# Kernel tuning notes

Measured on AMD Instinct MI355X. Metric: run time of the kernel, lower is better.

## Reference

```python
import jax, jax.numpy as jnp
import numpy as np
import math

B, C, H, W = 2, 64, 64, 64
DI = 2 * C          # d_inner
N = 16              # d_state
R = math.ceil(C / 16)  # dt_rank
K = 3               # d_conv
L = H * W

PARAM_KEYS = [
    'pe_x_w', 'pe_x_b', 'rms_x_w', 'conv_x_w', 'conv_x_b',
    'pe_info_w', 'pe_info_b', 'rms_info_w', 'conv_info_w', 'conv_info_b',
    'pe_mask_w', 'pe_mask_b', 'rms_mask_w', 'conv_mask_w', 'conv_mask_b',
    'in_x_w', 'in_info_w', 'in_mask_w',
    'delta_w', 'dt_w', 'dt_b', 'B_w', 'C_w', 'A_log', 'out_w',
]


def setup_inputs():
    key = jax.random.key(0)
    ki = iter(jax.random.split(key, 40))
    def nrm(shape, scale=1.0):
        return jax.random.normal(next(ki), shape, jnp.float32) * scale
    sc, sdi, sr, sk = 1/np.sqrt(C), 1/np.sqrt(DI), 1/np.sqrt(R), 1/np.sqrt(K)
    inp = {}
    for name in ('up', 'mask', 'x', 'y', 'z'):
        inp[name] = nrm((B, C, H, W))
    for role in ('x', 'info', 'mask'):
        inp[f'pe_{role}_w'] = nrm((3, C, C), sc)
        inp[f'pe_{role}_b'] = jnp.zeros((3, C), jnp.float32)
        inp[f'rms_{role}_w'] = jnp.ones((3, C), jnp.float32)
        inp[f'conv_{role}_w'] = nrm((3, DI, K), sk)
        inp[f'conv_{role}_b'] = nrm((3, DI), sk)
    inp['in_x_w'] = nrm((3, 2 * DI, C), sc)
    inp['in_info_w'] = nrm((3, DI, C), sc)
    inp['in_mask_w'] = nrm((3, DI, C), sc)
    inp['delta_w'] = nrm((3, R, DI), sdi)
    inp['dt_w'] = nrm((3, DI, R), sr)
    rng = np.random.default_rng(0)
    dt = np.exp(rng.uniform(size=(3, DI)) * (np.log(0.1) - np.log(0.001)) + np.log(0.001)).clip(min=1e-4)
    inp['dt_b'] = jnp.asarray(np.log(-np.expm1(-dt)), jnp.float32)
    inp['B_w'] = nrm((3, N, DI), sdi)
    inp['C_w'] = nrm((3, N, DI), sdi)
    inp['A_log'] = jnp.tile(jnp.log(jnp.arange(1, N + 1, dtype=jnp.float32)), (3, DI, 1))
    inp['out_w'] = nrm((3, C, DI), sdi)
    return inp


def embed1x1(t, w, b):
    # PatchEmbed with patch_size=1: 1x1 conv then flatten to [B, L, C]
    y = jnp.einsum('bchw,oc->bohw', t, w) + b[None, :, None, None]
    bb, cc, hh, ww = y.shape
    return y.reshape(bb, cc, hh * ww).transpose(0, 2, 1)


def rms_norm(x, w, eps=1e-5):
    return x * jax.lax.rsqrt(jnp.mean(x * x, axis=-1, keepdims=True) + eps) * w


def causal_dwconv_silu(x, w, b):
    # x [B, D, L]; depthwise causal conv1d (left-pad K-1), then SiLU
    kk = w.shape[1]
    xp = jnp.pad(x, ((0, 0), (0, 0), (kk - 1, 0)))
    y = jax.lax.conv_general_dilated(
        xp, w[:, None, :], window_strides=(1,), padding='VALID',
        dimension_numbers=('NCH', 'OIH', 'NCH'), feature_group_count=w.shape[0])
    return jax.nn.silu(y + b[None, :, None])


def selective_scan(u, delta, A, Bm, Cm):
    # u, delta: [B, D, L]; A: [D, N]; Bm, Cm: [B, N, L]
    dA = jnp.exp(jnp.einsum('bdl,dn->lbdn', delta, A))           # [L,B,D,N]
    dBu = jnp.einsum('bdl,bnl,bdl->lbdn', delta, Bm, u)          # [L,B,D,N]
    Ct = Cm.transpose(2, 0, 1)                                   # [L,B,N]
    h0 = jnp.zeros((u.shape[0], u.shape[1], A.shape[1]), u.dtype)
    def step(h, inp):
        dA_t, dBu_t, C_t = inp
        h = dA_t * h + dBu_t
        return h, jnp.einsum('bdn,bn->bd', h, C_t)
    _, ys = jax.lax.scan(step, h0, (dA, dBu, Ct))
    return ys.transpose(1, 2, 0)                                 # [B,D,L]


def branch(xin, maskin, upin, p):
    bb, cc, hh, ww = xin.shape
    xe = rms_norm(embed1x1(xin, p['pe_x_w'], p['pe_x_b']), p['rms_x_w'])        # [B,L,C]
    xz = jnp.einsum('blc,dc->bdl', xe, p['in_x_w'])                              # [B,2DI,L]
    di = xz.shape[1] // 2
    xc, x_act = xz[:, :di], xz[:, di:]
    info = rms_norm(embed1x1(upin, p['pe_info_w'], p['pe_info_b']), p['rms_info_w'])
    info = jnp.einsum('blc,dc->bdl', info, p['in_info_w'])
    mk = rms_norm(embed1x1(maskin, p['pe_mask_w'], p['pe_mask_b']), p['rms_mask_w'])
    mk = jnp.einsum('blc,dc->bdl', mk, p['in_mask_w'])
    xc = causal_dwconv_silu(xc, p['conv_x_w'], p['conv_x_b'])
    mk = causal_dwconv_silu(mk, p['conv_mask_w'], p['conv_mask_b'])
    info = causal_dwconv_silu(info, p['conv_info_w'], p['conv_info_b'])
    # S6: delta from mask, B from info, C from x
    delta = jnp.einsum('bdl,rd->brl', mk, p['delta_w'])
    delta = jnp.einsum('brl,dr->bdl', delta, p['dt_w'])
    delta = jax.nn.softplus(delta + p['dt_b'][None, :, None])
    A = -jnp.exp(p['A_log'])
    Bm = jnp.einsum('bdl,nd->bnl', info, p['B_w'])
    Cm = jnp.einsum('bdl,nd->bnl', xc, p['C_w'])
    y = selective_scan(xc, delta, A, Bm, Cm)
    y = y * jax.nn.silu(x_act)
    y = jnp.einsum('bdl,cd->blc', y, p['out_w'])
    return y.transpose(0, 2, 1).reshape(bb, cc, hh, ww) + xin


def forward(up, mask, x, y, z, *params):
    pall = dict(zip(PARAM_KEYS, params))
    out = None
    for i, feat in enumerate((x, y, z)):
        p = {k: v[i] for k, v in pall.items()}
        o = branch(feat, mask, up, p)
        out = o if out is None else out + o
    return out


def reference(up, mask, x, y, z,
              pe_x_w, pe_x_b, rms_x_w, conv_x_w, conv_x_b,
              pe_info_w, pe_info_b, rms_info_w, conv_info_w, conv_info_b,
              pe_mask_w, pe_mask_b, rms_mask_w, conv_mask_w, conv_mask_b,
              in_x_w, in_info_w, in_mask_w,
              delta_w, dt_w, dt_b, B_w, C_w, A_log, out_w):
    return forward(up, mask, x, y, z,
                   pe_x_w, pe_x_b, rms_x_w, conv_x_w, conv_x_b,
                   pe_info_w, pe_info_b, rms_info_w, conv_info_w, conv_info_b,
                   pe_mask_w, pe_mask_b, rms_mask_w, conv_mask_w, conv_mask_b,
                   in_x_w, in_info_w, in_mask_w,
                   delta_w, dt_w, dt_b, B_w, C_w, A_log, out_w)
```

## Files before the change

kernel.cpp:

```cpp
#include <hip/hip_runtime.h>
#include <math.h>

namespace {

constexpr int NB = 3;
constexpr int BB = 2;
constexpr int CC = 64;
constexpr int LLEN = 4096;
constexpr int DI = 128;
constexpr int NN = 16;
constexpr int RR = 4;
constexpr int GG = 256;
constexpr int LC = 16;
constexpr int NSEQ = NB * BB * DI * NN;
constexpr size_t SBUF = (size_t)NB * BB * DI * LLEN;

typedef _Float16 f16;
typedef __attribute__((ext_vector_type(4))) float f32x4;
typedef __attribute__((ext_vector_type(8))) short bf16x8;
typedef __attribute__((ext_vector_type(4))) _Float16 f16x4;
typedef __attribute__((ext_vector_type(8))) _Float16 f16x8;

__device__ __forceinline__ float siluf(float v) { return v / (1.f + __expf(-v)); }

__device__ __forceinline__ short cvt_bf16(float f) {
    union { float f; unsigned u; } v; v.f = f;
    unsigned r = v.u + 0x7fffu + ((v.u >> 16) & 1u);
    return (short)(r >> 16);
}
__device__ __forceinline__ unsigned pack_bf16(float lo, float hi) {
    return ((unsigned)(unsigned short)cvt_bf16(hi) << 16) | (unsigned short)cvt_bf16(lo);
}
__device__ __forceinline__ bf16x8 pack8(float4 a, float4 b) {
    bf16x8 r;
    r[0] = cvt_bf16(a.x); r[1] = cvt_bf16(a.y); r[2] = cvt_bf16(a.z); r[3] = cvt_bf16(a.w);
    r[4] = cvt_bf16(b.x); r[5] = cvt_bf16(b.y); r[6] = cvt_bf16(b.z); r[7] = cvt_bf16(b.w);
    return r;
}
__device__ __forceinline__ f16x4 to_h4(float a, float b, float c, float d) {
    f16x4 r; r[0] = (f16)a; r[1] = (f16)b; r[2] = (f16)c; r[3] = (f16)d; return r;
}
__device__ __forceinline__ float4 to_f4(f16x4 v) {
    return make_float4((float)v[0], (float)v[1], (float)v[2], (float)v[3]);
}
__device__ __forceinline__ int swz16(int l, int d) {
    int b = d >> 3;
    int bs = (b & 8) | ((b ^ l) & 7);
    return l * 128 + bs * 8 + (d & 7);
}

__global__ __launch_bounds__(256) void k1_embed(
    const float* __restrict__ up, const float* __restrict__ mask_,
    const float* __restrict__ fx, const float* __restrict__ fy, const float* __restrict__ fz,
    const float* __restrict__ pe_x_w, const float* __restrict__ pe_x_b, const float* __restrict__ rms_x_w,
    const float* __restrict__ pe_i_w, const float* __restrict__ pe_i_b, const float* __restrict__ rms_i_w,
    const float* __restrict__ pe_m_w, const float* __restrict__ pe_m_b, const float* __restrict__ rms_m_w,
    const float* __restrict__ in_x_w, const float* __restrict__ in_i_w, const float* __restrict__ in_m_w,
    f16* __restrict__ xc_pre, f16* __restrict__ x_act,
    f16* __restrict__ info_pre, f16* __restrict__ mk_pre)
{
    __shared__ short sE[64 * 64];
    __shared__ float red[4][64];
    __shared__ float sscl[64];

    int lt = blockIdx.x, job = blockIdx.y, b = blockIdx.z;
    int i = job / 3, r = job % 3;
    const float *src, *pw, *pb, *rw, *iw;
    if (r == 0) {
        src = (i == 0 ? fx : (i == 1 ? fy : fz));
        pw = pe_x_w + i * 4096; pb = pe_x_b + i * 64; rw = rms_x_w + i * 64;
        iw = in_x_w + (size_t)i * 256 * 64;
    } else if (r == 1) {
        src = up;
        pw = pe_i_w + i * 4096; pb = pe_i_b + i * 64; rw = rms_i_w + i * 64;
        iw = in_i_w + (size_t)i * 128 * 64;
    } else {
        src = mask_;
        pw = pe_m_w + i * 4096; pb = pe_m_b + i * 64; rw = rms_m_w + i * 64;
        iw = in_m_w + (size_t)i * 128 * 64;
    }
    int t = threadIdx.x;
    int w = t >> 6, lane = t & 63, lo = lane & 15, hi = lane >> 4;
    int l0 = lt * 64;
    const float* Xg = src + (size_t)b * 64 * LLEN;

    f32x4 acc1[4];
    #pragma unroll
    for (int nt = 0; nt < 4; ++nt) acc1[nt] = (f32x4){0.f, 0.f, 0.f, 0.f};

    #pragma unroll
    for (int ks = 0; ks < 2; ++ks) {
        const float* ap = pw + (16 * w + lo) * 64 + ks * 32 + hi * 8;
        bf16x8 a1 = pack8(*(const float4*)ap, *(const float4*)(ap + 4));
        #pragma unroll
        for (int nt = 0; nt < 4; ++nt) {
            const float* xc = Xg + (size_t)(ks * 32 + hi * 8) * LLEN + l0 + nt * 16 + lo;
            bf16x8 b1;
            #pragma unroll
            for (int j = 0; j < 8; ++j) b1[j] = cvt_bf16(xc[(size_t)j * LLEN]);
            acc1[nt] = __builtin_amdgcn_mfma_f32_16x16x32_bf16(a1, b1, acc1[nt], 0, 0, 0);
        }
    }

    float4 pbv = *(const float4*)&pb[16 * w + 4 * hi];
    float e_[4][4];
    #pragma unroll
    for (int nt = 0; nt < 4; ++nt) {
        e_[nt][0] = acc1[nt][0] + pbv.x;
        e_[nt][1] = acc1[nt][1] + pbv.y;
        e_[nt][2] = acc1[nt][2] + pbv.z;
        e_[nt][3] = acc1[nt][3] + pbv.w;
        float s = e_[nt][0] * e_[nt][0] + e_[nt][1] * e_[nt][1]
                + e_[nt][2] * e_[nt][2] + e_[nt][3] * e_[nt][3];
        s += __shfl_xor(s, 16);
        s += __shfl_xor(s, 32);
        if (lane < 16) red[w][nt * 16 + lo] = s;
    }
    __syncthreads();
    if (t < 64) {
        float s = red[0][t] + red[1][t] + red[2][t] + red[3][t];
        sscl[t] = rsqrtf(s * (1.f / 64.f) + 1e-5f);
    }
    __syncthreads();

    {
        int ob = 2 * w + (hi >> 1);
        #pragma unroll
        for (int nt = 0; nt < 4; ++nt) {
            float sc = sscl[16 * nt + lo];
            unsigned p0 = pack_bf16(e_[nt][0] * sc, e_[nt][1] * sc);
            unsigned p1 = pack_bf16(e_[nt][2] * sc, e_[nt][3] * sc);
            unsigned* p = (unsigned*)&sE[(16 * nt + lo) * 64 + (ob ^ (lo & 7)) * 8 + 4 * (hi & 1)];
            p[0] = p0; p[1] = p1;
        }
    }
    __syncthreads();

    bf16x8 b2[4][2];
    #pragma unroll
    for (int nt = 0; nt < 4; ++nt)
        #pragma unroll
        for (int ks = 0; ks < 2; ++ks) {
            int db = ks * 4 + hi;
            b2[nt][ks] = *(const bf16x8*)&sE[(16 * nt + lo) * 64 + (db ^ (lo & 7)) * 8];
        }

    size_t obase = ((size_t)(i * 2 + b)) * DI * LLEN;
    int MT = (r == 0) ? 4 : 2;
    for (int mm = 0; mm < MT; ++mm) {
        int m = MT * w + mm;
        bf16x8 a2[2];
        #pragma unroll
        for (int ks = 0; ks < 2; ++ks) {
            const float* wp = iw + (size_t)(16 * m + lo) * 64 + ks * 32 + hi * 8;
            float4 w0 = *(const float4*)wp;
            float4 w1 = *(const float4*)(wp + 4);
            float4 r0 = *(const float4*)&rw[ks * 32 + hi * 8];
            float4 r1 = *(const float4*)&rw[ks * 32 + hi * 8 + 4];
            w0.x *= r0.x; w0.y *= r0.y; w0.z *= r0.z; w0.w *= r0.w;
            w1.x *= r1.x; w1.y *= r1.y; w1.z *= r1.z; w1.w *= r1.w;
            a2[ks] = pack8(w0, w1);
        }
        f32x4 acc2[4];
        #pragma unroll
        for (int nt = 0; nt < 4; ++nt) acc2[nt] = (f32x4){0.f, 0.f, 0.f, 0.f};
        #pragma unroll
        for (int ks = 0; ks < 2; ++ks)
            #pragma unroll
            for (int nt = 0; nt < 4; ++nt)
                acc2[nt] = __builtin_amdgcn_mfma_f32_16x16x32_bf16(a2[ks], b2[nt][ks], acc2[nt], 0, 0, 0);

        int d0 = 16 * m + 4 * hi;
        f16* dst; int dd = d0;
        if (r == 0) { if (d0 < 128) dst = xc_pre; else { dst = x_act; dd = d0 - 128; } }
        else if (r == 1) dst = info_pre;
        else dst = mk_pre;
        #pragma unroll
        for (int nt = 0; nt < 4; ++nt) {
            int l = l0 + 16 * nt + lo;
            *(f16x4*)&dst[obase + (size_t)l * DI + dd] =
                to_h4(acc2[nt][0], acc2[nt][1], acc2[nt][2], acc2[nt][3]);
        }
    }
}

__global__ __launch_bounds__(256) void k3_conv(
    const f16* __restrict__ xc_pre, const f16* __restrict__ info_pre, const f16* __restrict__ mk_pre,
    const float* __restrict__ conv_x_w, const float* __restrict__ conv_x_b,
    const float* __restrict__ conv_i_w, const float* __restrict__ conv_i_b,
    const float* __restrict__ conv_m_w, const float* __restrict__ conv_m_b,
    const float* __restrict__ delta_w, const float* __restrict__ dt_w, const float* __restrict__ dt_b,
    const float* __restrict__ B_w, const float* __restrict__ C_w,
    f16* __restrict__ u, f16* __restrict__ delta,
    f16* __restrict__ Bm, f16* __restrict__ Cm)
{
    __shared__ __align__(16) f16 ot[64 * 128];
    __shared__ float rvec[4 * 64];

    int lt = blockIdx.x, ib = blockIdx.y, strm = blockIdx.z;
    int i = ib >> 1;
    int t = threadIdx.x;
    int l0 = lt * 64;
    size_t base = (size_t)ib * DI * LLEN;

    const f16 *inb; const float *cw, *cb;
    if (strm == 0)      { inb = mk_pre;   cw = conv_m_w + i * DI * 3; cb = conv_m_b + i * DI; }
    else if (strm == 1) { inb = info_pre; cw = conv_i_w + i * DI * 3; cb = conv_i_b + i * DI; }
    else                { inb = xc_pre;   cw = conv_x_w + i * DI * 3; cb = conv_x_b + i * DI; }

    {
        int d4 = t & 31, lq = t >> 5;
        int d = d4 * 4;
        float cw0[4], cw1[4], cw2[4], cbb[4];
        #pragma unroll
        for (int j = 0; j < 4; ++j) {
            cw0[j] = cw[(d + j) * 3 + 0];
            cw1[j] = cw[(d + j) * 3 + 1];
            cw2[j] = cw[(d + j) * 3 + 2];
            cbb[j] = cb[d + j];
        }
        int gl0 = l0 + lq * 8;
        float4 x0 = make_float4(0.f, 0.f, 0.f, 0.f), x1 = x0;
        if (gl0 >= 2) x0 = to_f4(*(const f16x4*)&inb[base + (size_t)(gl0 - 2) * DI + d]);
        if (gl0 >= 1) x1 = to_f4(*(const f16x4*)&inb[base + (size_t)(gl0 - 1) * DI + d]);
        #pragma unroll
        for (int li = 0; li < 8; ++li) {
            int l = lq * 8 + li;
            float4 x2 = to_f4(*(const f16x4*)&inb[base + (size_t)(gl0 + li) * DI + d]);
            float4 v;
            v.x = siluf(cw0[0] * x0.x + cw1[0] * x1.x + cw2[0] * x2.x + cbb[0]);
            v.y = siluf(cw0[1] * x0.y + cw1[1] * x1.y + cw2[1] * x2.y + cbb[1]);
            v.z = siluf(cw0[2] * x0.z + cw1[2] * x1.z + cw2[2] * x2.z + cbb[2]);
            v.w = siluf(cw0[3] * x0.w + cw1[3] * x1.w + cw2[3] * x2.w + cbb[3]);
            f16x4 hv = to_h4(v.x, v.y, v.z, v.w);
            *(f16x4*)&ot[swz16(l, d)] = hv;
            if (strm == 2) *(f16x4*)&u[base + (size_t)(gl0 + li) * DI + d] = hv;
            x0 = x1; x1 = x2;
        }
    }
    __syncthreads();

    if (strm == 0) {
        {
            int l = t & 63, r = t >> 6;
            const float* dw = delta_w + i * RR * DI + r * DI;
            float acc = 0.f;
            #pragma unroll
            for (int db = 0; db < 16; ++db) {
                f16x8 v = *(const f16x8*)&ot[swz16(l, db * 8)];
                int d0 = db * 8;
                #pragma unroll
                for (int j = 0; j < 8; ++j) acc += dw[d0 + j] * (float)v[j];
            }
            rvec[r * 64 + l] = acc;
        }
        __syncthreads();
        {
            int d = t & 127, lh = t >> 7;
            const float* dtw = dt_w + i * DI * RR + d * RR;
            float w0 = dtw[0], w1 = dtw[1], w2 = dtw[2], w3 = dtw[3];
            float bb = dt_b[i * DI + d];
            #pragma unroll 4
            for (int li = 0; li < 32; ++li) {
                int l = lh * 32 + li;
                float v = bb + w0 * rvec[l] + w1 * rvec[64 + l] + w2 * rvec[128 + l] + w3 * rvec[192 + l];
                float sp = (v > 20.f) ? v : log1pf(__expf(v));
                delta[base + (size_t)(l0 + l) * DI + d] = (f16)sp;
            }
        }
    } else {
        int l = t & 63, ng = t >> 6;
        const float* wv = ((strm == 1) ? B_w : C_w) + i * NN * DI + ng * 4 * DI;
        float a0 = 0.f, a1 = 0.f, a2 = 0.f, a3 = 0.f;
        #pragma unroll
        for (int db = 0; db < 16; ++db) {
            f16x8 v = *(const f16x8*)&ot[swz16(l, db * 8)];
            int d0 = db * 8;
            #pragma unroll
            for (int j = 0; j < 8; ++j) {
                float x = (float)v[j];
                a0 += wv[d0 + j] * x;
                a1 += wv[DI + d0 + j] * x;
                a2 += wv[2 * DI + d0 + j] * x;
                a3 += wv[3 * DI + d0 + j] * x;
            }
        }
        f16* dst = (strm == 1) ? Bm : Cm;
        *(f16x4*)&dst[((size_t)ib * LLEN + l0 + l) * NN + ng * 4] = to_h4(a0, a1, a2, a3);
    }
}

__global__ __launch_bounds__(128) void k4_scan1(
    const f16* __restrict__ u, const f16* __restrict__ delta,
    const f16* __restrict__ Bm, const float* __restrict__ A_log,
    f16* __restrict__ aprod, f16* __restrict__ hend)
{
    __shared__ __align__(16) float sB[LC * 16];
    int g = blockIdx.x, ib = blockIdx.y, i = ib >> 1;
    int d = threadIdx.x;
    if (d < 64) {
        f16x4 v = ((const f16x4*)(Bm + ((size_t)ib * LLEN + (size_t)g * LC) * NN))[d];
        ((float4*)sB)[d] = to_f4(v);
    }
    float A[16], h[16];
    {
        const float4* al = (const float4*)(A_log + ((size_t)i * DI + d) * NN);
        #pragma unroll
        for (int q = 0; q < 4; ++q) {
            float4 v = al[q];
            A[4 * q] = -__expf(v.x); A[4 * q + 1] = -__expf(v.y);
            A[4 * q + 2] = -__expf(v.z); A[4 * q + 3] = -__expf(v.w);
        }
    }
    #pragma unroll
    for (int n = 0; n < 16; ++n) h[n] = 0.f;
    float sdl = 0.f;
    __syncthreads();
    size_t base = ((size_t)ib * LLEN + (size_t)g * LC) * DI + d;
    #pragma unroll 4
    for (int li = 0; li < LC; ++li) {
        float dl = (float)delta[base + li * DI];
        float du = dl * (float)u[base + li * DI];
        sdl += dl;
        const float4* bl = (const float4*)(sB + li * 16);
        float4 b0 = bl[0], b1 = bl[1], b2 = bl[2], b3 = bl[3];
        h[0] = __expf(dl * A[0]) * h[0] + du * b0.x;  h[1] = __expf(dl * A[1]) * h[1] + du * b0.y;
        h[2] = __expf(dl * A[2]) * h[2] + du * b0.z;  h[3] = __expf(dl * A[3]) * h[3] + du * b0.w;
        h[4] = __expf(dl * A[4]) * h[4] + du * b1.x;  h[5] = __expf(dl * A[5]) * h[5] + du * b1.y;
        h[6] = __expf(dl * A[6]) * h[6] + du * b1.z;  h[7] = __expf(dl * A[7]) * h[7] + du * b1.w;
        h[8] = __expf(dl * A[8]) * h[8] + du * b2.x;  h[9] = __expf(dl * A[9]) * h[9] + du * b2.y;
        h[10] = __expf(dl * A[10]) * h[10] + du * b2.z; h[11] = __expf(dl * A[11]) * h[11] + du * b2.w;
        h[12] = __expf(dl * A[12]) * h[12] + du * b3.x; h[13] = __expf(dl * A[13]) * h[13] + du * b3.y;
        h[14] = __expf(dl * A[14]) * h[14] + du * b3.z; h[15] = __expf(dl * A[15]) * h[15] + du * b3.w;
    }
    size_t seq = ((size_t)ib * DI + d) * NN;
    f16x8* ap = (f16x8*)(aprod + (size_t)g * NSEQ + seq);
    f16x8* he = (f16x8*)(hend + (size_t)g * NSEQ + seq);
    #pragma unroll
    for (int q = 0; q < 2; ++q) {
        f16x8 av, hv;
        #pragma unroll
        for (int j = 0; j < 8; ++j) {
            av[j] = (f16)__expf(A[8 * q + j] * sdl);
            hv[j] = (f16)h[8 * q + j];
        }
        ap[q] = av; he[q] = hv;
    }
}

__global__ __launch_bounds__(256) void k5_prefix(
    const f16* __restrict__ aprod, const f16* __restrict__ hend,
    f16* __restrict__ hin)
{
    int s = blockIdx.x * 256 + threadIdx.x;
    float h = 0.f;
    #pragma unroll 8
    for (int g = 0; g < GG; ++g) {
        hin[(size_t)g * NSEQ + s] = (f16)h;
        h = (float)aprod[(size_t)g * NSEQ + s] * h + (float)hend[(size_t)g * NSEQ + s];
    }
}

__global__ __launch_bounds__(128) void k6_scan2(
    const f16* __restrict__ u, const f16* __restrict__ delta,
    const f16* __restrict__ Bm, const f16* __restrict__ Cm,
    const float* __restrict__ A_log, const f16* __restrict__ hin,
    f16* __restrict__ y)
{
    __shared__ __align__(16) float sB[LC * 16];
    __shared__ __align__(16) float sC[LC * 16];
    int g = blockIdx.x, ib = blockIdx.y, i = ib >> 1;
    int d = threadIdx.x;
    {
        const f16x4* bsrc = (const f16x4*)(Bm + ((size_t)ib * LLEN + (size_t)g * LC) * NN);
        const f16x4* csrc = (const f16x4*)(Cm + ((size_t)ib * LLEN + (size_t)g * LC) * NN);
        if (d < 64) ((float4*)sB)[d] = to_f4(bsrc[d]);
        else ((float4*)sC)[d - 64] = to_f4(csrc[d - 64]);
    }
    float A[16], h[16];
    {
        const float4* al = (const float4*)(A_log + ((size_t)i * DI + d) * NN);
        #pragma unroll
        for (int q = 0; q < 4; ++q) {
            float4 v = al[q];
            A[4 * q] = -__expf(v.x); A[4 * q + 1] = -__expf(v.y);
            A[4 * q + 2] = -__expf(v.z); A[4 * q + 3] = -__expf(v.w);
        }
    }
    {
        size_t seq = ((size_t)ib * DI + d) * NN;
        const f16x8* hp = (const f16x8*)(hin + (size_t)g * NSEQ + seq);
        #pragma unroll
        for (int q = 0; q < 2; ++q) {
            f16x8 v = hp[q];
            #pragma unroll
            for (int j = 0; j < 8; ++j) h[8 * q + j] = (float)v[j];
        }
    }
    __syncthreads();
    size_t base = ((size_t)ib * LLEN + (size_t)g * LC) * DI + d;
    #pragma unroll 4
    for (int li = 0; li < LC; ++li) {
        float dl = (float)delta[base + li * DI];
        float du = dl * (float)u[base + li * DI];
        const float4* bl = (const float4*)(sB + li * 16);
        const float4* cl = (const float4*)(sC + li * 16);
        float4 b0 = bl[0], b1 = bl[1], b2 = bl[2], b3 = bl[3];
        float4 c0 = cl[0], c1 = cl[1], c2 = cl[2], c3 = cl[3];
        float acc = 0.f;
        h[0] = __expf(dl * A[0]) * h[0] + du * b0.x;  acc += h[0] * c0.x;
        h[1] = __expf(dl * A[1]) * h[1] + du * b0.y;  acc += h[1] * c0.y;
        h[2] = __expf(dl * A[2]) * h[2] + du * b0.z;  acc += h[2] * c0.z;
        h[3] = __expf(dl * A[3]) * h[3] + du * b0.w;  acc += h[3] * c0.w;
        h[4] = __expf(dl * A[4]) * h[4] + du * b1.x;  acc += h[4] * c1.x;
        h[5] = __expf(dl * A[5]) * h[5] + du * b1.y;  acc += h[5] * c1.y;
        h[6] = __expf(dl * A[6]) * h[6] + du * b1.z;  acc += h[6] * c1.z;
        h[7] = __expf(dl * A[7]) * h[7] + du * b1.w;  acc += h[7] * c1.w;
        h[8] = __expf(dl * A[8]) * h[8] + du * b2.x;  acc += h[8] * c2.x;
        h[9] = __expf(dl * A[9]) * h[9] + du * b2.y;  acc += h[9] * c2.y;
        h[10] = __expf(dl * A[10]) * h[10] + du * b2.z; acc += h[10] * c2.z;
        h[11] = __expf(dl * A[11]) * h[11] + du * b2.w; acc += h[11] * c2.w;
        h[12] = __expf(dl * A[12]) * h[12] + du * b3.x; acc += h[12] * c3.x;
        h[13] = __expf(dl * A[13]) * h[13] + du * b3.y; acc += h[13] * c3.y;
        h[14] = __expf(dl * A[14]) * h[14] + du * b3.z; acc += h[14] * c3.z;
        h[15] = __expf(dl * A[15]) * h[15] + du * b3.w; acc += h[15] * c3.w;
        y[base + li * DI] = (f16)acc;
    }
}

__global__ __launch_bounds__(256) void k7_out(
    const f16* __restrict__ y, const f16* __restrict__ xact,
    const float* __restrict__ out_w,
    const float* __restrict__ fx, const float* __restrict__ fy, const float* __restrict__ fz,
    float* __restrict__ out)
{
    __shared__ short sG[64 * 128];
    int lt = blockIdx.x, b = blockIdx.y;
    int l0 = lt * 64;
    int t = threadIdx.x;
    int w = t >> 6, lane = t & 63, lo = lane & 15, hi = lane >> 4;

    f32x4 acc[4];
    #pragma unroll
    for (int nt = 0; nt < 4; ++nt) acc[nt] = (f32x4){0.f, 0.f, 0.f, 0.f};

    for (int i = 0; i < 3; ++i) {
        size_t base = ((size_t)(i * 2 + b)) * DI * LLEN;
        __syncthreads();
        #pragma unroll
        for (int p = 0; p < 8; ++p) {
            int idx = t + 256 * p;
            int d4 = idx & 31, l = idx >> 5;
            int d = d4 * 4;
            float4 yv = to_f4(*(const f16x4*)&y[base + (size_t)(l0 + l) * DI + d]);
            float4 xa = to_f4(*(const f16x4*)&xact[base + (size_t)(l0 + l) * DI + d]);
            float g0 = yv.x * siluf(xa.x), g1 = yv.y * siluf(xa.y);
            float g2 = yv.z * siluf(xa.z), g3 = yv.w * siluf(xa.w);
            int blk = d4 >> 1;
            int blks = (blk & 8) | ((blk ^ (l & 7)) & 7);
            unsigned* p32 = (unsigned*)&sG[l * 128 + blks * 8 + 4 * (d4 & 1)];
            p32[0] = pack_bf16(g0, g1);
            p32[1] = pack_bf16(g2, g3);
        }
        __syncthreads();

        const float* ow = out_w + (size_t)i * CC * DI;
        bf16x8 a[4];
        #pragma unroll
        for (int ks = 0; ks < 4; ++ks) {
            const float* ap = ow + (size_t)(16 * w + lo) * 128 + ks * 32 + hi * 8;
            a[ks] = pack8(*(const float4*)ap, *(const float4*)(ap + 4));
        }
        #pragma unroll
        for (int nt = 0; nt < 4; ++nt) {
            int l = 16 * nt + lo;
            #pragma unroll
            for (int ks = 0; ks < 4; ++ks) {
                int db = ks * 4 + hi;
                int blks = (db & 8) | ((db ^ (l & 7)) & 7);
                bf16x8 bv = *(const bf16x8*)&sG[l * 128 + blks * 8];
                acc[nt] = __builtin_amdgcn_mfma_f32_16x16x32_bf16(a[ks], bv, acc[nt], 0, 0, 0);
            }
        }
    }

    #pragma unroll
    for (int nt = 0; nt < 4; ++nt) {
        int l = l0 + 16 * nt + lo;
        int cbase = 16 * w + 4 * hi;
        #pragma unroll
        for (int rr = 0; rr < 4; ++rr) {
            int c = cbase + rr;
            size_t idx = ((size_t)b * CC + c) * LLEN + l;
            out[idx] = acc[nt][rr] + fx[idx] + fy[idx] + fz[idx];
        }
    }
}

}

extern "C" void kernel_launch(void* const* d_in, const int* in_sizes, int n_in,
                              void* d_out, int out_size, void* d_ws, size_t ws_size,
                              hipStream_t stream)
{
    (void)in_sizes; (void)n_in; (void)out_size; (void)ws_size;
    const float* up       = (const float*)d_in[0];
    const float* mask_    = (const float*)d_in[1];
    const float* fx       = (const float*)d_in[2];
    const float* fy       = (const float*)d_in[3];
    const float* fz       = (const float*)d_in[4];
    const float* pe_x_w   = (const float*)d_in[5];
    const float* pe_x_b   = (const float*)d_in[6];
    const float* rms_x_w  = (const float*)d_in[7];
    const float* conv_x_w = (const float*)d_in[8];
    const float* conv_x_b = (const float*)d_in[9];
    const float* pe_i_w   = (const float*)d_in[10];
    const float* pe_i_b   = (const float*)d_in[11];
    const float* rms_i_w  = (const float*)d_in[12];
    const float* conv_i_w = (const float*)d_in[13];
    const float* conv_i_b = (const float*)d_in[14];
    const float* pe_m_w   = (const float*)d_in[15];
    const float* pe_m_b   = (const float*)d_in[16];
    const float* rms_m_w  = (const float*)d_in[17];
    const float* conv_m_w = (const float*)d_in[18];
    const float* conv_m_b = (const float*)d_in[19];
    const float* in_x_w   = (const float*)d_in[20];
    const float* in_i_w   = (const float*)d_in[21];
    const float* in_m_w   = (const float*)d_in[22];
    const float* delta_w  = (const float*)d_in[23];
    const float* dt_w     = (const float*)d_in[24];
    const float* dt_b     = (const float*)d_in[25];
    const float* B_w      = (const float*)d_in[26];
    const float* C_w      = (const float*)d_in[27];
    const float* A_log    = (const float*)d_in[28];
    const float* out_w    = (const float*)d_in[29];
    float* out = (float*)d_out;

    f16* ws = (f16*)d_ws;
    const size_t S = SBUF;
    f16* xc_pre   = ws;
    f16* x_act    = ws + S;
    f16* info_pre = ws + 2 * S;
    f16* mk_pre   = ws + 3 * S;
    f16* ubuf     = ws + 4 * S;
    f16* dbuf     = ws + 5 * S;
    f16* BmB      = ws + 6 * S;
    f16* CmB      = BmB + (size_t)NB * BB * NN * LLEN;
    f16* aprod = info_pre;
    f16* hendb = mk_pre;
    f16* hinb  = xc_pre;
    f16* ybuf  = info_pre;

    hipLaunchKernelGGL(k1_embed, dim3(64, 9, 2), dim3(256), 0, stream,
        up, mask_, fx, fy, fz,
        pe_x_w, pe_x_b, rms_x_w, pe_i_w, pe_i_b, rms_i_w, pe_m_w, pe_m_b, rms_m_w,
        in_x_w, in_i_w, in_m_w, xc_pre, x_act, info_pre, mk_pre);

    hipLaunchKernelGGL(k3_conv, dim3(64, 6, 3), dim3(256), 0, stream,
        xc_pre, info_pre, mk_pre,
        conv_x_w, conv_x_b, conv_i_w, conv_i_b, conv_m_w, conv_m_b,
        delta_w, dt_w, dt_b, B_w, C_w, ubuf, dbuf, BmB, CmB);

    hipLaunchKernelGGL(k4_scan1, dim3(GG, 6), dim3(128), 0, stream,
        ubuf, dbuf, BmB, A_log, aprod, hendb);

    hipLaunchKernelGGL(k5_prefix, dim3(NSEQ / 256), dim3(256), 0, stream,
        aprod, hendb, hinb);

    hipLaunchKernelGGL(k6_scan2, dim3(GG, 6), dim3(128), 0, stream,
        ubuf, dbuf, BmB, CmB, A_log, hinb, ybuf);

    hipLaunchKernelGGL(k7_out, dim3(64, 2), dim3(256), 0, stream,
        ybuf, x_act, out_w, fx, fy, fz, out);
}
```

Baseline: 127.3 us.

## Fuse chunked scan phases into one cooperative kernel with grid syncs

Merges the three scan phases (per-chunk local scan, cross-chunk prefix, final scan with output) into a single cooperative kernel that uses grid.sync between phases, with the old three-launch path kept as a fallback. The goal is to remove two kernel launch boundaries and let the final phase reuse the B/C tiles in shared memory and the A values in registers. The trade-off is that the prefix phase now runs on only 128 threads per block across 1536 blocks. Grid-wide barriers and cooperative launch limits can also add overhead or make the launch fail if not all blocks fit on the device at once.

```diff
diff --git a/kernel.cpp b/kernel.cpp
--- a/kernel.cpp
+++ b/kernel.cpp
@@ -1,5 +1,8 @@
 #include <hip/hip_runtime.h>
+#include <hip/hip_cooperative_groups.h>
 #include <math.h>
+
+namespace cg = cooperative_groups;
 
 namespace {
 
@@ -290,6 +293,127 @@
     }
 }
 
+#define SCAN_STEP_NOACC(dl, du, b0, b1, b2, b3)                                  \
+    h[0] = __expf((dl) * A[0]) * h[0] + (du) * b0.x;                             \
+    h[1] = __expf((dl) * A[1]) * h[1] + (du) * b0.y;                             \
+    h[2] = __expf((dl) * A[2]) * h[2] + (du) * b0.z;                             \
+    h[3] = __expf((dl) * A[3]) * h[3] + (du) * b0.w;                             \
+    h[4] = __expf((dl) * A[4]) * h[4] + (du) * b1.x;                             \
+    h[5] = __expf((dl) * A[5]) * h[5] + (du) * b1.y;                             \
+    h[6] = __expf((dl) * A[6]) * h[6] + (du) * b1.z;                             \
+    h[7] = __expf((dl) * A[7]) * h[7] + (du) * b1.w;                             \
+    h[8] = __expf((dl) * A[8]) * h[8] + (du) * b2.x;                             \
+    h[9] = __expf((dl) * A[9]) * h[9] + (du) * b2.y;                             \
+    h[10] = __expf((dl) * A[10]) * h[10] + (du) * b2.z;                          \
+    h[11] = __expf((dl) * A[11]) * h[11] + (du) * b2.w;                          \
+    h[12] = __expf((dl) * A[12]) * h[12] + (du) * b3.x;                          \
+    h[13] = __expf((dl) * A[13]) * h[13] + (du) * b3.y;                          \
+    h[14] = __expf((dl) * A[14]) * h[14] + (du) * b3.z;                          \
+    h[15] = __expf((dl) * A[15]) * h[15] + (du) * b3.w;
+
+__global__ __launch_bounds__(128) void k46_scan(
+    const f16* __restrict__ u, const f16* __restrict__ delta,
+    const f16* __restrict__ Bm, const f16* __restrict__ Cm,
+    const float* __restrict__ A_log,
+    f16* __restrict__ aprod, f16* __restrict__ hend,
+    f16* __restrict__ hin, f16* __restrict__ y)
+{
+    __shared__ __align__(16) float sB[LC * 16];
+    __shared__ __align__(16) float sC[LC * 16];
+    cg::grid_group grid = cg::this_grid();
+
+    int g = blockIdx.x, ib = blockIdx.y, i = ib >> 1;
+    int d = threadIdx.x;
+    {
+        const f16x4* bsrc = (const f16x4*)(Bm + ((size_t)ib * LLEN + (size_t)g * LC) * NN);
+        const f16x4* csrc = (const f16x4*)(Cm + ((size_t)ib * LLEN + (size_t)g * LC) * NN);
+        if (d < 64) ((float4*)sB)[d] = to_f4(bsrc[d]);
+        else ((float4*)sC)[d - 64] = to_f4(csrc[d - 64]);
+    }
+    float A[16], h[16];
+    {
+        const float4* al = (const float4*)(A_log + ((size_t)i * DI + d) * NN);
+        #pragma unroll
+        for (int q = 0; q < 4; ++q) {
+            float4 v = al[q];
+            A[4 * q] = -__expf(v.x); A[4 * q + 1] = -__expf(v.y);
+            A[4 * q + 2] = -__expf(v.z); A[4 * q + 3] = -__expf(v.w);
+        }
+    }
+    #pragma unroll
+    for (int n = 0; n < 16; ++n) h[n] = 0.f;
+    float sdl = 0.f;
+    __syncthreads();
+
+    size_t base = ((size_t)ib * LLEN + (size_t)g * LC) * DI + d;
+    #pragma unroll 4
+    for (int li = 0; li < LC; ++li) {
+        float dl = (float)delta[base + li * DI];
+        float du = dl * (float)u[base + li * DI];
+        sdl += dl;
+        const float4* bl = (const float4*)(sB + li * 16);
+        float4 b0 = bl[0], b1 = bl[1], b2 = bl[2], b3 = bl[3];
+        SCAN_STEP_NOACC(dl, du, b0, b1, b2, b3)
+    }
+    size_t seq = ((size_t)ib * DI + d) * NN;
+    {
+        f16x8* ap = (f16x8*)(aprod + (size_t)g * NSEQ + seq);
+        f16x8* he = (f16x8*)(hend + (size_t)g * NSEQ + seq);
+        #pragma unroll
+        for (int q = 0; q < 2; ++q) {
+            f16x8 av, hv;
+            #pragma unroll
+            for (int j = 0; j < 8; ++j) {
+                av[j] = (f16)__expf(A[8 * q + j] * sdl);
+                hv[j] = (f16)h[8 * q + j];
+            }
+            ap[q] = av; he[q] = hv;
+        }
+    }
+
+    grid.sync();
+
+    {
+        int flat = blockIdx.y * (int)gridDim.x + blockIdx.x;
+        int s = flat * 128 + (int)threadIdx.x;
+        if (s < NSEQ) {
+            float hh = 0.f;
+            #pragma unroll 8
+            for (int gg = 0; gg < GG; ++gg) {
+                hin[(size_t)gg * NSEQ + s] = (f16)hh;
+                hh = (float)aprod[(size_t)gg * NSEQ + s] * hh + (float)hend[(size_t)gg * NSEQ + s];
+            }
+        }
+    }
+
+    grid.sync();
+
+    {
+        const f16x8* hp = (const f16x8*)(hin + (size_t)g * NSEQ + seq);
+        #pragma unroll
+        for (int q = 0; q < 2; ++q) {
+            f16x8 v = hp[q];
+            #pragma unroll
+            for (int j = 0; j < 8; ++j) h[8 * q + j] = (float)v[j];
+        }
+    }
+    #pragma unroll 4
+    for (int li = 0; li < LC; ++li) {
+        float dl = (float)delta[base + li * DI];
+        float du = dl * (float)u[base + li * DI];
+        const float4* bl = (const float4*)(sB + li * 16);
+        const float4* cl = (const float4*)(sC + li * 16);
+        float4 b0 = bl[0], b1 = bl[1], b2 = bl[2], b3 = bl[3];
+        float4 c0 = cl[0], c1 = cl[1], c2 = cl[2], c3 = cl[3];
+        SCAN_STEP_NOACC(dl, du, b0, b1, b2, b3)
+        float acc = h[0] * c0.x + h[1] * c0.y + h[2] * c0.z + h[3] * c0.w
+                  + h[4] * c1.x + h[5] * c1.y + h[6] * c1.z + h[7] * c1.w
+                  + h[8] * c2.x + h[9] * c2.y + h[10] * c2.z + h[11] * c2.w
+                  + h[12] * c3.x + h[13] * c3.y + h[14] * c3.z + h[15] * c3.w;
+        y[base + li * DI] = (f16)acc;
+    }
+}
+
 __global__ __launch_bounds__(128) void k4_scan1(
     const f16* __restrict__ u, const f16* __restrict__ delta,
     const f16* __restrict__ Bm, const float* __restrict__ A_log,
@@ -324,14 +448,7 @@
         sdl += dl;
         const float4* bl = (const float4*)(sB + li * 16);
         float4 b0 = bl[0], b1 = bl[1], b2 = bl[2], b3 = bl[3];
-        h[0] = __expf(dl * A[0]) * h[0] + du * b0.x;  h[1] = __expf(dl * A[1]) * h[1] + du * b0.y;
-        h[2] = __expf(dl * A[2]) * h[2] + du * b0.z;  h[3] = __expf(dl * A[3]) * h[3] + du * b0.w;
-        h[4] = __expf(dl * A[4]) * h[4] + du * b1.x;  h[5] = __expf(dl * A[5]) * h[5] + du * b1.y;
-        h[6] = __expf(dl * A[6]) * h[6] + du * b1.z;  h[7] = __expf(dl * A[7]) * h[7] + du * b1.w;
-        h[8] = __expf(dl * A[8]) * h[8] + du * b2.x;  h[9] = __expf(dl * A[9]) * h[9] + du * b2.y;
-        h[10] = __expf(dl * A[10]) * h[10] + du * b2.z; h[11] = __expf(dl * A[11]) * h[11] + du * b2.w;
-        h[12] = __expf(dl * A[12]) * h[12] + du * b3.x; h[13] = __expf(dl * A[13]) * h[13] + du * b3.y;
-        h[14] = __expf(dl * A[14]) * h[14] + du * b3.z; h[15] = __expf(dl * A[15]) * h[15] + du * b3.w;
+        SCAN_STEP_NOACC(dl, du, b0, b1, b2, b3)
     }
     size_t seq = ((size_t)ib * DI + d) * NN;
     f16x8* ap = (f16x8*)(aprod + (size_t)g * NSEQ + seq);
@@ -407,23 +524,11 @@
         const float4* cl = (const float4*)(sC + li * 16);
         float4 b0 = bl[0], b1 = bl[1], b2 = bl[2], b3 = bl[3];
         float4 c0 = cl[0], c1 = cl[1], c2 = cl[2], c3 = cl[3];
-        float acc = 0.f;
-        h[0] = __expf(dl * A[0]) * h[0] + du * b0.x;  acc += h[0] * c0.x;
-        h[1] = __expf(dl * A[1]) * h[1] + du * b0.y;  acc += h[1] * c0.y;
-        h[2] = __expf(dl * A[2]) * h[2] + du * b0.z;  acc += h[2] * c0.z;
-        h[3] = __expf(dl * A[3]) * h[3] + du * b0.w;  acc += h[3] * c0.w;
-        h[4] = __expf(dl * A[4]) * h[4] + du * b1.x;  acc += h[4] * c1.x;
-        h[5] = __expf(dl * A[5]) * h[5] + du * b1.y;  acc += h[5] * c1.y;
-        h[6] = __expf(dl * A[6]) * h[6] + du * b1.z;  acc += h[6] * c1.z;
-        h[7] = __expf(dl * A[7]) * h[7] + du * b1.w;  acc += h[7] * c1.w;
-        h[8] = __expf(dl * A[8]) * h[8] + du * b2.x;  acc += h[8] * c2.x;
-        h[9] = __expf(dl * A[9]) * h[9] + du * b2.y;  acc += h[9] * c2.y;
-        h[10] = __expf(dl * A[10]) * h[10] + du * b2.z; acc += h[10] * c2.z;
-        h[11] = __expf(dl * A[11]) * h[11] + du * b2.w; acc += h[11] * c2.w;
-        h[12] = __expf(dl * A[12]) * h[12] + du * b3.x; acc += h[12] * c3.x;
-        h[13] = __expf(dl * A[13]) * h[13] + du * b3.y; acc += h[13] * c3.y;
-        h[14] = __expf(dl * A[14]) * h[14] + du * b3.z; acc += h[14] * c3.z;
-        h[15] = __expf(dl * A[15]) * h[15] + du * b3.w; acc += h[15] * c3.w;
+        SCAN_STEP_NOACC(dl, du, b0, b1, b2, b3)
+        float acc = h[0] * c0.x + h[1] * c0.y + h[2] * c0.z + h[3] * c0.w
+                  + h[4] * c1.x + h[5] * c1.y + h[6] * c1.z + h[7] * c1.w
+                  + h[8] * c2.x + h[9] * c2.y + h[10] * c2.z + h[11] * c2.w
+                  + h[12] * c3.x + h[13] * c3.y + h[14] * c3.z + h[15] * c3.w;
         y[base + li * DI] = (f16)acc;
     }
 }
@@ -561,14 +666,24 @@
         conv_x_w, conv_x_b, conv_i_w, conv_i_b, conv_m_w, conv_m_b,
         delta_w, dt_w, dt_b, B_w, C_w, ubuf, dbuf, BmB, CmB);
 
-    hipLaunchKernelGGL(k4_scan1, dim3(GG, 6), dim3(128), 0, stream,
-        ubuf, dbuf, BmB, A_log, aprod, hendb);
-
-    hipLaunchKernelGGL(k5_prefix, dim3(NSEQ / 256), dim3(256), 0, stream,
-        aprod, hendb, hinb);
-
-    hipLaunchKernelGGL(k6_scan2, dim3(GG, 6), dim3(128), 0, stream,
-        ubuf, dbuf, BmB, CmB, A_log, hinb, ybuf);
+    hipError_t ce;
+    {
+        const f16* a_u = ubuf; const f16* a_d = dbuf;
+        const f16* a_B = BmB;  const f16* a_C = CmB;
+        const float* a_A = A_log;
+        f16* a_ap = aprod; f16* a_he = hendb; f16* a_hi = hinb; f16* a_y = ybuf;
+        void* args[] = { &a_u, &a_d, &a_B, &a_C, &a_A, &a_ap, &a_he, &a_hi, &a_y };
+        ce = hipLaunchCooperativeKernel((const void*)k46_scan, dim3(GG, 6), dim3(128),
+                                        args, 0, stream);
+    }
+    if (ce != hipSuccess) {
+        hipLaunchKernelGGL(k4_scan1, dim3(GG, 6), dim3(128), 0, stream,
+            ubuf, dbuf, BmB, A_log, aprod, hendb);
+        hipLaunchKernelGGL(k5_prefix, dim3(NSEQ / 256), dim3(256), 0, stream,
+            aprod, hendb, hinb);
+        hipLaunchKernelGGL(k6_scan2, dim3(GG, 6), dim3(128), 0, stream,
+            ubuf, dbuf, BmB, CmB, A_log, hinb, ybuf);
+    }
 
     hipLaunchKernelGGL(k7_out, dim3(64, 2), dim3(256), 0, stream,
         ybuf, x_act, out_w, fx, fy, fz, out);
```

Result: slower. 411.8 us (+223.5%).
